# Kernel optimization log

Measured on AMD Instinct MI355X. Metric: run time of the kernel, lower is better.

Reference implementation:

```python
import jax, jax.numpy as jnp
import numpy as np

N_NODES = 100000
N_EDGES = 1000000
H = 128


def setup_inputs() -> dict:
    key = jax.random.key(0)
    ks = jax.random.split(key, 8)
    s = 1.0 / np.sqrt(H)
    return {
        "x": jax.random.normal(ks[0], (N_NODES, H), dtype=jnp.float32),
        "edge_index": jax.random.randint(ks[1], (2, N_EDGES), 0, N_NODES, dtype=jnp.int64),
        "W_p": jax.random.normal(ks[2], (H, H), dtype=jnp.float32) * s,
        "b_p": jnp.zeros((H,), dtype=jnp.float32),
        "W_c": jax.random.normal(ks[3], (H, H), dtype=jnp.float32) * s,
        "b_c": jnp.zeros((H,), dtype=jnp.float32),
        "W1": jax.random.normal(ks[4], (3 * H, H), dtype=jnp.float32) * (1.0 / np.sqrt(3 * H)),
        "b1": jnp.zeros((H,), dtype=jnp.float32),
        "W2": jax.random.normal(ks[5], (H, 1), dtype=jnp.float32) * s,
        "b2": jnp.zeros((1,), dtype=jnp.float32),
    }


def reference(x, edge_index, W_p, b_p, W_c, b_c, W1, b1, W2, b2):
    # Gather parent (src) and child (dst) node features per edge: [E, H]
    par_fea = x[edge_index[0]]
    cld_fea = x[edge_index[1]]
    # Dual small MLPs (LeakyReLU slope 0.01, dropout inactive at inference)
    enc_p = jax.nn.leaky_relu(par_fea @ W_p + b_p, negative_slope=0.01)
    enc_c = jax.nn.leaky_relu(cld_fea @ W_c + b_c, negative_slope=0.01)
    diff = jnp.abs(par_fea - cld_fea)
    edge_features = jnp.concatenate([enc_p, enc_c, diff], axis=-1)  # [E, 3H]
    h = jax.nn.relu(edge_features @ W1 + b1)
    edge_weight = jax.nn.sigmoid(h @ W2 + b2).squeeze(-1)  # [E]
    return edge_weight
```

## Files before the change

kernel.cpp:

```cpp
#include <hip/hip_runtime.h>
#include <hip/hip_bf16.h>

#define E_EDGES 1000000
#define N_NODES 100000
#define HDIM 128
#define BM 64
#define LDP 136

typedef __attribute__((ext_vector_type(8))) short short8;
typedef __attribute__((ext_vector_type(4))) float f32x4;

static __device__ __forceinline__ short f2bf(float f) {
  unsigned int u = __float_as_uint(f);
  unsigned int r = (u + 0x7FFFu + ((u >> 16) & 1u)) >> 16;
  return (short)r;
}
static __device__ __forceinline__ float bf2f(short s) {
  return __uint_as_float(((unsigned int)(unsigned short)s) << 16);
}
static __device__ __forceinline__ unsigned int pack_bf16_rn(float lo, float hi) {
  __hip_bfloat162 h = __float22bfloat162_rn(make_float2(lo, hi));
  unsigned int u;
  __builtin_memcpy(&u, &h, 4);
  return u;
}

__global__ void prep_weights(const float* __restrict__ Wp, const float* __restrict__ Wc,
                             const float* __restrict__ W1, const float* __restrict__ W2,
                             short* __restrict__ wp_t, short* __restrict__ wc_t,
                             short* __restrict__ w1_t, float* __restrict__ w2v) {
  int i = blockIdx.x * 256 + threadIdx.x;
  if (i < HDIM * HDIM) {
    int o = i >> 7, k = i & (HDIM - 1);
    wp_t[i] = f2bf(Wp[k * HDIM + o]);
    wc_t[i] = f2bf(Wc[k * HDIM + o]);
  }
  if (i < HDIM * 3 * HDIM) {
    int o = i / (3 * HDIM), k = i - o * (3 * HDIM);
    w1_t[i] = f2bf(W1[k * HDIM + o]);
  }
  if (i < HDIM) w2v[i] = W2[i];
}

__global__ __launch_bounds__(256) void node_precompute(
    const float* __restrict__ x, const float* __restrict__ b_p,
    const float* __restrict__ b_c, const float* __restrict__ b1,
    const short* __restrict__ wp_t, const short* __restrict__ wc_t,
    const short* __restrict__ w1_t,
    short* __restrict__ x_bf, short* __restrict__ Abuf, short* __restrict__ Bbuf) {
  __shared__ __align__(16) short Xt[BM * LDP];
  __shared__ __align__(16) short Yp[BM * LDP];
  __shared__ __align__(16) short Yc[BM * LDP];

  const int t = threadIdx.x;
  const int n0 = blockIdx.x * BM;

  {
    const int lane16 = t & 15, rq = t >> 4, c0 = lane16 * 8;
#pragma unroll
    for (int pass = 0; pass < 4; ++pass) {
      const int row = pass * 16 + rq;
      const int n = n0 + row;
      short8 v;
      if (n < N_NODES) {
        const float* ps = x + (size_t)n * HDIM + c0;
        float4 a = *(const float4*)ps;
        float4 b = *(const float4*)(ps + 4);
        float f[8] = {a.x, a.y, a.z, a.w, b.x, b.y, b.z, b.w};
#pragma unroll
        for (int j = 0; j < 8; ++j) v[j] = f2bf(f[j]);
        *(short8*)&x_bf[(size_t)n * HDIM + c0] = v;
      } else {
#pragma unroll
        for (int j = 0; j < 8; ++j) v[j] = 0;
      }
      *(short8*)&Xt[row * LDP + c0] = v;
    }
  }
  __syncthreads();

  const int l = t & 63;
  const int w = t >> 6;
  const int lr = l & 15;
  const int lg = l >> 4;
  const int aoff = lr * LDP + lg * 8;
  const int na = w * 32 + lr, nb = na + 16;

  const f32x4 zero4 = {0.f, 0.f, 0.f, 0.f};
  f32x4 ap_[4][2], ac_[4][2];
#pragma unroll
  for (int mi = 0; mi < 4; ++mi) {
    ap_[mi][0] = zero4; ap_[mi][1] = zero4;
    ac_[mi][0] = zero4; ac_[mi][1] = zero4;
  }

  const short* wpA = wp_t + na * HDIM + lg * 8;
  const short* wpB = wp_t + nb * HDIM + lg * 8;
  const short* wcA = wc_t + na * HDIM + lg * 8;
  const short* wcB = wc_t + nb * HDIM + lg * 8;

#pragma unroll
  for (int kk = 0; kk < 4; ++kk) {
    short8 b10 = *(const short8*)(wpA + kk * 32);
    short8 b11 = *(const short8*)(wpB + kk * 32);
    short8 b20 = *(const short8*)(wcA + kk * 32);
    short8 b21 = *(const short8*)(wcB + kk * 32);
#pragma unroll
    for (int mi = 0; mi < 4; ++mi) {
      short8 a8 = *(const short8*)&Xt[mi * 16 * LDP + aoff + kk * 32];
      ap_[mi][0] = __builtin_amdgcn_mfma_f32_16x16x32_bf16(a8, b10, ap_[mi][0], 0, 0, 0);
      ap_[mi][1] = __builtin_amdgcn_mfma_f32_16x16x32_bf16(a8, b11, ap_[mi][1], 0, 0, 0);
      ac_[mi][0] = __builtin_amdgcn_mfma_f32_16x16x32_bf16(a8, b20, ac_[mi][0], 0, 0, 0);
      ac_[mi][1] = __builtin_amdgcn_mfma_f32_16x16x32_bf16(a8, b21, ac_[mi][1], 0, 0, 0);
    }
  }

  {
    const float bpa = b_p[na], bpb = b_p[nb];
    const float bca = b_c[na], bcb = b_c[nb];
#pragma unroll
    for (int mi = 0; mi < 4; ++mi) {
#pragma unroll
      for (int r = 0; r < 4; ++r) {
        const int m = mi * 16 + lg * 4 + r;
        float v0 = ap_[mi][0][r] + bpa; v0 = v0 > 0.f ? v0 : 0.01f * v0;
        float v1 = ap_[mi][1][r] + bpb; v1 = v1 > 0.f ? v1 : 0.01f * v1;
        float u0 = ac_[mi][0][r] + bca; u0 = u0 > 0.f ? u0 : 0.01f * u0;
        float u1 = ac_[mi][1][r] + bcb; u1 = u1 > 0.f ? u1 : 0.01f * u1;
        Yp[m * LDP + na] = f2bf(v0);
        Yp[m * LDP + nb] = f2bf(v1);
        Yc[m * LDP + na] = f2bf(u0);
        Yc[m * LDP + nb] = f2bf(u1);
      }
    }
  }
  __syncthreads();

  f32x4 aa_[4][2], ab_[4][2];
#pragma unroll
  for (int mi = 0; mi < 4; ++mi) {
    aa_[mi][0] = zero4; aa_[mi][1] = zero4;
    ab_[mi][0] = zero4; ab_[mi][1] = zero4;
  }
  const short* w1Aa = w1_t + na * (3 * HDIM) + lg * 8;
  const short* w1Ab = w1_t + nb * (3 * HDIM) + lg * 8;
#pragma unroll
  for (int kk = 0; kk < 4; ++kk) {
    short8 ba0 = *(const short8*)(w1Aa + kk * 32);
    short8 ba1 = *(const short8*)(w1Ab + kk * 32);
    short8 bb0 = *(const short8*)(w1Aa + HDIM + kk * 32);
    short8 bb1 = *(const short8*)(w1Ab + HDIM + kk * 32);
#pragma unroll
    for (int mi = 0; mi < 4; ++mi) {
      short8 ayp = *(const short8*)&Yp[mi * 16 * LDP + aoff + kk * 32];
      short8 ayc = *(const short8*)&Yc[mi * 16 * LDP + aoff + kk * 32];
      aa_[mi][0] = __builtin_amdgcn_mfma_f32_16x16x32_bf16(ayp, ba0, aa_[mi][0], 0, 0, 0);
      aa_[mi][1] = __builtin_amdgcn_mfma_f32_16x16x32_bf16(ayp, ba1, aa_[mi][1], 0, 0, 0);
      ab_[mi][0] = __builtin_amdgcn_mfma_f32_16x16x32_bf16(ayc, bb0, ab_[mi][0], 0, 0, 0);
      ab_[mi][1] = __builtin_amdgcn_mfma_f32_16x16x32_bf16(ayc, bb1, ab_[mi][1], 0, 0, 0);
    }
  }

  {
    const float b1a = b1[na], b1b = b1[nb];
#pragma unroll
    for (int mi = 0; mi < 4; ++mi) {
#pragma unroll
      for (int r = 0; r < 4; ++r) {
        const int m = mi * 16 + lg * 4 + r;
        const int n = n0 + m;
        if (n < N_NODES) {
          Abuf[(size_t)n * HDIM + na] = f2bf(aa_[mi][0][r] + b1a);
          Abuf[(size_t)n * HDIM + nb] = f2bf(aa_[mi][1][r] + b1b);
          Bbuf[(size_t)n * HDIM + na] = f2bf(ab_[mi][0][r]);
          Bbuf[(size_t)n * HDIM + nb] = f2bf(ab_[mi][1][r]);
        }
      }
    }
  }
}

__global__ __launch_bounds__(512, 8) void edge_kernel(
    const int* __restrict__ ei, const short* __restrict__ x_bf,
    const short* __restrict__ Abuf, const short* __restrict__ Bbuf,
    const short* __restrict__ w1_t, const float* __restrict__ w2v,
    const float* __restrict__ b2, float* __restrict__ out) {
  __shared__ __align__(16) short Dt[BM * LDP];
  __shared__ __align__(16) short St[BM * LDP];
  __shared__ float partial[8][BM];

  const int t = threadIdx.x;
  const int e0 = blockIdx.x * BM;

  {
    const int lane16 = t & 15, rq = t >> 4, c0 = lane16 * 8;
#pragma unroll
    for (int pass = 0; pass < 2; ++pass) {
      const int row = pass * 32 + rq;
      const int s = ei[e0 + row];
      const int d = ei[E_EDGES + e0 + row];
      short8 p8 = *(const short8*)(x_bf + (size_t)s * HDIM + c0);
      short8 c8 = *(const short8*)(x_bf + (size_t)d * HDIM + c0);
      short8 a8 = *(const short8*)(Abuf + (size_t)s * HDIM + c0);
      short8 b8 = *(const short8*)(Bbuf + (size_t)d * HDIM + c0);
      float df[8], sf[8];
#pragma unroll
      for (int j = 0; j < 8; ++j) {
        df[j] = fabsf(bf2f(p8[j]) - bf2f(c8[j]));
        sf[j] = bf2f(a8[j]) + bf2f(b8[j]);
      }
      uint4 vd, vs;
      vd.x = pack_bf16_rn(df[0], df[1]);
      vd.y = pack_bf16_rn(df[2], df[3]);
      vd.z = pack_bf16_rn(df[4], df[5]);
      vd.w = pack_bf16_rn(df[6], df[7]);
      vs.x = pack_bf16_rn(sf[0], sf[1]);
      vs.y = pack_bf16_rn(sf[2], sf[3]);
      vs.z = pack_bf16_rn(sf[4], sf[5]);
      vs.w = pack_bf16_rn(sf[6], sf[7]);
      *(uint4*)&Dt[row * LDP + c0] = vd;
      *(uint4*)&St[row * LDP + c0] = vs;
    }
  }
  __syncthreads();

  const int l = t & 63;
  const int w = t >> 6;
  const int lr = l & 15;
  const int lg = l >> 4;
  const int na = w * 16 + lr;
  const int aoff = lr * LDP + lg * 8;

  f32x4 acc[4];
#pragma unroll
  for (int mi = 0; mi < 4; ++mi) {
#pragma unroll
    for (int r = 0; r < 4; ++r) {
      acc[mi][r] = bf2f(St[(mi * 16 + lg * 4 + r) * LDP + na]);
    }
  }

  const short* w1D = w1_t + na * (3 * HDIM) + 2 * HDIM + lg * 8;
#pragma unroll
  for (int kk = 0; kk < 4; ++kk) {
    short8 b8 = *(const short8*)(w1D + kk * 32);
#pragma unroll
    for (int mi = 0; mi < 4; ++mi) {
      short8 a8 = *(const short8*)&Dt[mi * 16 * LDP + aoff + kk * 32];
      acc[mi] = __builtin_amdgcn_mfma_f32_16x16x32_bf16(a8, b8, acc[mi], 0, 0, 0);
    }
  }

  {
    const float w2a = w2v[na];
#pragma unroll
    for (int mi = 0; mi < 4; ++mi) {
#pragma unroll
      for (int r = 0; r < 4; ++r) {
        float h = acc[mi][r] > 0.f ? acc[mi][r] : 0.f;
        float v = h * w2a;
        v += __shfl_xor(v, 1);
        v += __shfl_xor(v, 2);
        v += __shfl_xor(v, 4);
        v += __shfl_xor(v, 8);
        if (lr == 0) partial[w][mi * 16 + lg * 4 + r] = v;
      }
    }
  }
  __syncthreads();

  if (t < BM) {
    float z = partial[0][t] + partial[1][t] + partial[2][t] + partial[3][t] +
              partial[4][t] + partial[5][t] + partial[6][t] + partial[7][t] + b2[0];
    out[e0 + t] = 1.0f / (1.0f + __expf(-z));
  }
}

__global__ __launch_bounds__(512, 4) void edge_weight_fallback(
    const float* __restrict__ x, const int* __restrict__ ei,
    const float* __restrict__ b_p, const float* __restrict__ b_c,
    const float* __restrict__ b1, const float* __restrict__ b2,
    const short* __restrict__ wp_t, const short* __restrict__ wc_t,
    const short* __restrict__ w1_t, const float* __restrict__ w2v,
    float* __restrict__ out) {
  __shared__ __align__(16) short Pt[BM * LDP];
  __shared__ __align__(16) short Ct[BM * LDP];
  __shared__ __align__(16) short Dt[BM * LDP];
  __shared__ float partial[8][BM];

  const int t = threadIdx.x;
  const int e0 = blockIdx.x * BM;
  {
    const int lane16 = t & 15, rq = t >> 4, c0 = lane16 * 8;
#pragma unroll
    for (int pass = 0; pass < 2; ++pass) {
      const int row = pass * 32 + rq;
      const int ip = ei[e0 + row];
      const int ic = ei[E_EDGES + e0 + row];
      const float* ps = x + (size_t)ip * HDIM + c0;
      const float* cs = x + (size_t)ic * HDIM + c0;
      float4 pa = *(const float4*)ps, pb = *(const float4*)(ps + 4);
      float4 ca = *(const float4*)cs, cb = *(const float4*)(cs + 4);
      float pf[8] = {pa.x, pa.y, pa.z, pa.w, pb.x, pb.y, pb.z, pb.w};
      float cf[8] = {ca.x, ca.y, ca.z, ca.w, cb.x, cb.y, cb.z, cb.w};
      short8 vp, vc, vd;
#pragma unroll
      for (int j = 0; j < 8; ++j) {
        vp[j] = f2bf(pf[j]); vc[j] = f2bf(cf[j]); vd[j] = f2bf(fabsf(pf[j] - cf[j]));
      }
      *(short8*)&Pt[row * LDP + c0] = vp;
      *(short8*)&Ct[row * LDP + c0] = vc;
      *(short8*)&Dt[row * LDP + c0] = vd;
    }
  }
  __syncthreads();
  const int l = t & 63, w = t >> 6, lr = l & 15, lg = l >> 4;
  const int n0 = w * 16, na = n0 + lr, aoff = lr * LDP + lg * 8;
  const f32x4 zero4 = {0.f, 0.f, 0.f, 0.f};
  f32x4 acc1[4], acc2[4], acc3[4];
#pragma unroll
  for (int mi = 0; mi < 4; ++mi) { acc1[mi] = zero4; acc2[mi] = zero4; acc3[mi] = zero4; }
  const short* wpA = wp_t + na * HDIM + lg * 8;
  const short* wcA = wc_t + na * HDIM + lg * 8;
  const short* w1A = w1_t + na * (3 * HDIM) + lg * 8;
#pragma unroll
  for (int kk = 0; kk < 4; ++kk) {
    short8 bp8 = *(const short8*)(wpA + kk * 32);
    short8 bc8 = *(const short8*)(wcA + kk * 32);
    short8 bd8 = *(const short8*)(w1A + 2 * HDIM + kk * 32);
#pragma unroll
    for (int mi = 0; mi < 4; ++mi) {
      short8 ap = *(const short8*)&Pt[mi * 16 * LDP + aoff + kk * 32];
      short8 ac = *(const short8*)&Ct[mi * 16 * LDP + aoff + kk * 32];
      short8 ad = *(const short8*)&Dt[mi * 16 * LDP + aoff + kk * 32];
      acc1[mi] = __builtin_amdgcn_mfma_f32_16x16x32_bf16(ap, bp8, acc1[mi], 0, 0, 0);
      acc2[mi] = __builtin_amdgcn_mfma_f32_16x16x32_bf16(ac, bc8, acc2[mi], 0, 0, 0);
      acc3[mi] = __builtin_amdgcn_mfma_f32_16x16x32_bf16(ad, bd8, acc3[mi], 0, 0, 0);
    }
  }
  __syncthreads();
  {
    const float bpa = b_p[na], bca = b_c[na];
#pragma unroll
    for (int mi = 0; mi < 4; ++mi) {
#pragma unroll
      for (int r = 0; r < 4; ++r) {
        const int m = mi * 16 + lg * 4 + r;
        float v0 = acc1[mi][r] + bpa; v0 = v0 > 0.f ? v0 : 0.01f * v0;
        float u0 = acc2[mi][r] + bca; u0 = u0 > 0.f ? u0 : 0.01f * u0;
        Pt[m * LDP + na] = f2bf(v0);
        Ct[m * LDP + na] = f2bf(u0);
      }
    }
  }
  __syncthreads();
#pragma unroll
  for (int kk = 0; kk < 4; ++kk) {
    short8 b0 = *(const short8*)(w1A + kk * 32);
    short8 b1f = *(const short8*)(w1A + HDIM + kk * 32);
#pragma unroll
    for (int mi = 0; mi < 4; ++mi) {
      short8 a0 = *(const short8*)&Pt[mi * 16 * LDP + aoff + kk * 32];
      short8 a1 = *(const short8*)&Ct[mi * 16 * LDP + aoff + kk * 32];
      acc3[mi] = __builtin_amdgcn_mfma_f32_16x16x32_bf16(a0, b0, acc3[mi], 0, 0, 0);
      acc3[mi] = __builtin_amdgcn_mfma_f32_16x16x32_bf16(a1, b1f, acc3[mi], 0, 0, 0);
    }
  }
  {
    const float b1a = b1[na], w2a = w2v[na];
#pragma unroll
    for (int mi = 0; mi < 4; ++mi) {
#pragma unroll
      for (int r = 0; r < 4; ++r) {
        float h0 = acc3[mi][r] + b1a; h0 = h0 > 0.f ? h0 : 0.f;
        float v = h0 * w2a;
        v += __shfl_xor(v, 1); v += __shfl_xor(v, 2);
        v += __shfl_xor(v, 4); v += __shfl_xor(v, 8);
        if (lr == 0) partial[w][mi * 16 + lg * 4 + r] = v;
      }
    }
  }
  __syncthreads();
  if (t < BM) {
    float z = partial[0][t] + partial[1][t] + partial[2][t] + partial[3][t] +
              partial[4][t] + partial[5][t] + partial[6][t] + partial[7][t] + b2[0];
    out[e0 + t] = 1.0f / (1.0f + __expf(-z));
  }
}

extern "C" void kernel_launch(void* const* d_in, const int* in_sizes, int n_in,
                              void* d_out, int out_size, void* d_ws, size_t ws_size,
                              hipStream_t stream) {
  const float* x  = (const float*)d_in[0];
  const int*   ei = (const int*)d_in[1];
  const float* Wp = (const float*)d_in[2];
  const float* bp = (const float*)d_in[3];
  const float* Wc = (const float*)d_in[4];
  const float* bc = (const float*)d_in[5];
  const float* W1 = (const float*)d_in[6];
  const float* b1 = (const float*)d_in[7];
  const float* W2 = (const float*)d_in[8];
  const float* b2 = (const float*)d_in[9];
  float* out = (float*)d_out;

  short* wp_t = (short*)d_ws;
  short* wc_t = wp_t + HDIM * HDIM;
  short* w1_t = wc_t + HDIM * HDIM;
  float* w2v  = (float*)(w1_t + HDIM * 3 * HDIM);
  short* x_bf = (short*)(w2v + HDIM);
  short* Abuf = x_bf + (size_t)N_NODES * HDIM;
  short* Bbuf = Abuf + (size_t)N_NODES * HDIM;

  const size_t needed = (size_t)((char*)(Bbuf + (size_t)N_NODES * HDIM) - (char*)d_ws);

  prep_weights<<<(HDIM * 3 * HDIM + 255) / 256, 256, 0, stream>>>(Wp, Wc, W1, W2,
                                                                  wp_t, wc_t, w1_t, w2v);
  if (ws_size >= needed) {
    node_precompute<<<(N_NODES + BM - 1) / BM, 256, 0, stream>>>(
        x, bp, bc, b1, wp_t, wc_t, w1_t, x_bf, Abuf, Bbuf);
    edge_kernel<<<E_EDGES / BM, 512, 0, stream>>>(ei, x_bf, Abuf, Bbuf, w1_t, w2v, b2, out);
  } else {
    edge_weight_fallback<<<E_EDGES / BM, 512, 0, stream>>>(x, ei, bp, bc, b1, b2,
                                                           wp_t, wc_t, w1_t, w2v, out);
  }
}
```

Baseline: 216.3 us.

## Bucket-sort edges by source node and remap blocks per XCD for gather locality

Adds a histogram, scan and atomic scatter pass that builds a permutation grouping edges by source-node bucket (128 nodes per bucket). The edge kernel processes edges in that order and writes results back through the permutation. Block IDs are also remapped so each XCD works on a contiguous range, so source-row gathers (x_bf and Abuf) should hit in the per-XCD L2. The cost is three extra kernel launches, a memset, atomic contention in the scatter pass and scattered output writes.

```diff
diff --git a/kernel.cpp b/kernel.cpp
--- a/kernel.cpp
+++ b/kernel.cpp
@@ -6,6 +6,7 @@
 #define HDIM 128
 #define BM 64
 #define LDP 136
+#define NB 1024
 
 typedef __attribute__((ext_vector_type(8))) short short8;
 typedef __attribute__((ext_vector_type(4))) float f32x4;
@@ -40,6 +41,50 @@
     w1_t[i] = f2bf(W1[k * HDIM + o]);
   }
   if (i < HDIM) w2v[i] = W2[i];
+}
+
+__global__ __launch_bounds__(512) void hist_kernel(const int* __restrict__ ei,
+                                                   int* __restrict__ hist) {
+  __shared__ int h[NB];
+  const int t = threadIdx.x;
+  h[t] = 0; h[t + 512] = 0;
+  __syncthreads();
+  const int base = blockIdx.x * 2048;
+#pragma unroll
+  for (int i = 0; i < 4; ++i) {
+    int e = base + i * 512 + t;
+    if (e < E_EDGES) atomicAdd(&h[ei[e] >> 7], 1);
+  }
+  __syncthreads();
+  if (h[t]) atomicAdd(&hist[t], h[t]);
+  if (h[t + 512]) atomicAdd(&hist[t + 512], h[t + 512]);
+}
+
+__global__ __launch_bounds__(NB) void scan_kernel(const int* __restrict__ hist,
+                                                  int* __restrict__ cursor) {
+  __shared__ int s[NB];
+  const int t = threadIdx.x;
+  const int my = hist[t];
+  s[t] = my;
+  __syncthreads();
+  for (int off = 1; off < NB; off <<= 1) {
+    int v = (t >= off) ? s[t - off] : 0;
+    __syncthreads();
+    s[t] += v;
+    __syncthreads();
+  }
+  cursor[t] = s[t] - my;
+}
+
+__global__ __launch_bounds__(512) void scatter_kernel(const int* __restrict__ ei,
+                                                      int* __restrict__ cursor,
+                                                      int* __restrict__ perm) {
+  int e = blockIdx.x * 512 + threadIdx.x;
+  if (e < E_EDGES) {
+    int b = ei[e] >> 7;
+    int pos = atomicAdd(&cursor[b], 1);
+    perm[pos] = e;
+  }
 }
 
 __global__ __launch_bounds__(256) void node_precompute(
@@ -181,24 +226,35 @@
 }
 
 __global__ __launch_bounds__(512, 8) void edge_kernel(
-    const int* __restrict__ ei, const short* __restrict__ x_bf,
-    const short* __restrict__ Abuf, const short* __restrict__ Bbuf,
-    const short* __restrict__ w1_t, const float* __restrict__ w2v,
-    const float* __restrict__ b2, float* __restrict__ out) {
+    const int* __restrict__ ei, const int* __restrict__ perm,
+    const short* __restrict__ x_bf, const short* __restrict__ Abuf,
+    const short* __restrict__ Bbuf, const short* __restrict__ w1_t,
+    const float* __restrict__ w2v, const float* __restrict__ b2,
+    float* __restrict__ out, int nblocks) {
   __shared__ __align__(16) short Dt[BM * LDP];
   __shared__ __align__(16) short St[BM * LDP];
   __shared__ float partial[8][BM];
-
+  __shared__ int eidS[BM];
+
+  int bid = blockIdx.x;
+  {
+    const int nx = 8;
+    const int q = nblocks / nx, r = nblocks % nx;
+    const int xcd = bid % nx, idx = bid / nx;
+    bid = (xcd < r ? xcd * (q + 1) : r * (q + 1) + (xcd - r) * q) + idx;
+  }
   const int t = threadIdx.x;
-  const int e0 = blockIdx.x * BM;
+  const int e0 = bid * BM;
 
   {
     const int lane16 = t & 15, rq = t >> 4, c0 = lane16 * 8;
 #pragma unroll
     for (int pass = 0; pass < 2; ++pass) {
       const int row = pass * 32 + rq;
-      const int s = ei[e0 + row];
-      const int d = ei[E_EDGES + e0 + row];
+      const int eidx = perm ? perm[e0 + row] : (e0 + row);
+      eidS[row] = eidx;
+      const int s = ei[eidx];
+      const int d = ei[E_EDGES + eidx];
       short8 p8 = *(const short8*)(x_bf + (size_t)s * HDIM + c0);
       short8 c8 = *(const short8*)(x_bf + (size_t)d * HDIM + c0);
       short8 a8 = *(const short8*)(Abuf + (size_t)s * HDIM + c0);
@@ -272,7 +328,7 @@
   if (t < BM) {
     float z = partial[0][t] + partial[1][t] + partial[2][t] + partial[3][t] +
               partial[4][t] + partial[5][t] + partial[6][t] + partial[7][t] + b2[0];
-    out[e0 + t] = 1.0f / (1.0f + __expf(-z));
+    out[eidS[t]] = 1.0f / (1.0f + __expf(-z));
   }
 }
 
@@ -410,17 +466,31 @@
   short* x_bf = (short*)(w2v + HDIM);
   short* Abuf = x_bf + (size_t)N_NODES * HDIM;
   short* Bbuf = Abuf + (size_t)N_NODES * HDIM;
-
-  const size_t needed = (size_t)((char*)(Bbuf + (size_t)N_NODES * HDIM) - (char*)d_ws);
+  int*   hist = (int*)(Bbuf + (size_t)N_NODES * HDIM);
+  int*   cursor = hist + NB;
+  int*   perm = cursor + NB;
+
+  const size_t needed_tables = (size_t)((char*)hist - (char*)d_ws);
+  const size_t needed_sort   = (size_t)((char*)(perm + E_EDGES) - (char*)d_ws);
+  const int nblocks = E_EDGES / BM;
 
   prep_weights<<<(HDIM * 3 * HDIM + 255) / 256, 256, 0, stream>>>(Wp, Wc, W1, W2,
                                                                   wp_t, wc_t, w1_t, w2v);
-  if (ws_size >= needed) {
+  if (ws_size >= needed_tables) {
     node_precompute<<<(N_NODES + BM - 1) / BM, 256, 0, stream>>>(
         x, bp, bc, b1, wp_t, wc_t, w1_t, x_bf, Abuf, Bbuf);
-    edge_kernel<<<E_EDGES / BM, 512, 0, stream>>>(ei, x_bf, Abuf, Bbuf, w1_t, w2v, b2, out);
+    const int* perm_arg = nullptr;
+    if (ws_size >= needed_sort) {
+      hipMemsetAsync(hist, 0, NB * sizeof(int), stream);
+      hist_kernel<<<(E_EDGES + 2047) / 2048, 512, 0, stream>>>(ei, hist);
+      scan_kernel<<<1, NB, 0, stream>>>(hist, cursor);
+      scatter_kernel<<<(E_EDGES + 511) / 512, 512, 0, stream>>>(ei, cursor, perm);
+      perm_arg = perm;
+    }
+    edge_kernel<<<nblocks, 512, 0, stream>>>(ei, perm_arg, x_bf, Abuf, Bbuf,
+                                             w1_t, w2v, b2, out, nblocks);
   } else {
-    edge_weight_fallback<<<E_EDGES / BM, 512, 0, stream>>>(x, ei, bp, bc, b1, b2,
-                                                           wp_t, wc_t, w1_t, w2v, out);
-  }
-}
+    edge_weight_fallback<<<nblocks, 512, 0, stream>>>(x, ei, bp, bc, b1, b2,
+                                                      wp_t, wc_t, w1_t, w2v, out);
+  }
+}
```

After: 473.6 us. 119% more time.
